# Optimization experiments

Hardware: AMD Instinct MI355X
Metric: run time of the kernel (lower is better)

## Reference

```python
import jax, jax.numpy as jnp
import numpy as np

N_ATOMS = 64
N_SAMPLES = 2 ** 15
SAMPLERATE = 22050
N_RES = 4096
N_ROOMS = 8
N_COEFFS = N_SAMPLES // 2 + 1


def make_waves():
    # musical_scale_hz(21, 106, 4096//4) -> 4 waveform families (sine, saw, square, triangle)
    n_steps = N_RES // 4
    midi = np.linspace(21.0, 106.0, n_steps)
    f0 = 440.0 * 2.0 ** ((midi - 69.0) / 12.0)
    rps = ((f0 / (SAMPLERATE / 2.0)) * np.pi).astype(np.float32)
    rad = rps[:, None] * np.arange(N_SAMPLES, dtype=np.float32)[None, :]
    sine = np.sin(rad)
    t = rad / (2.0 * np.pi)
    saw = (2.0 * (t - np.floor(t + 0.5))).astype(np.float32)
    sq = np.sign(sine).astype(np.float32)
    tri = (2.0 * np.abs(saw) - 1.0).astype(np.float32)
    return jnp.asarray(np.concatenate([sine, saw, sq, tri], 0).reshape(1, N_RES, N_SAMPLES))


def pdf2(means, stds, n):
    # gaussian pdf evaluated on linspace(0,1,n); means/stds: (1, A)
    rng = jnp.linspace(0.0, 1.0, n)
    mu = means[..., None]
    sd = stds[..., None]
    return jnp.exp(-0.5 * ((rng - mu) / sd) ** 2) / (sd * jnp.sqrt(2.0 * jnp.pi))


def linear_interp(x, n_out):
    # F.interpolate(mode='linear', align_corners=False) on last axis; x: (b, a, f)
    f = x.shape[-1]
    pos = (jnp.arange(n_out) + 0.5) * (f / n_out) - 0.5
    pos = jnp.clip(pos, 0.0, f - 1)
    i0 = jnp.floor(pos).astype(jnp.int32)
    i1 = jnp.minimum(i0 + 1, f - 1)
    w = (pos - i0).astype(x.dtype)
    return x[..., i0] * (1.0 - w) + x[..., i1] * w


def exponential_decay(decay_values, n_atoms, n_frames, base_resonance, n_samples):
    dv = jax.nn.sigmoid(decay_values.reshape(-1, n_atoms, 1))
    dv = jnp.broadcast_to(dv, (dv.shape[0], n_atoms, n_frames))
    decay = base_resonance + dv * (1.0 - base_resonance) * 0.95
    decay = jnp.exp(jnp.cumsum(jnp.log(decay + 1e-12), axis=-1))
    return linear_interp(decay, n_samples)


def fft_convolve(a, b):
    # zero-pad to 2N, multiply spectra, take first N samples
    n = a.shape[-1]
    pa = jnp.pad(a, ((0, 0), (0, 0), (0, n)))
    pb = jnp.pad(b, ((0, 0), (0, 0), (0, n)))
    spec = jnp.fft.rfft(pa, axis=-1) * jnp.fft.rfft(pb, axis=-1)
    return jnp.fft.irfft(spec, n=2 * n, axis=-1)[..., :n]


def layer_norm(x, w, b, eps=1e-5):
    m = jnp.mean(x, axis=-1, keepdims=True)
    v = jnp.var(x, axis=-1, keepdims=True)
    return (x - m) / jnp.sqrt(v + eps) * w + b


def sparse_softmax_st(x):
    soft = jax.nn.softmax(x, axis=-1)
    hard = jax.nn.one_hot(jnp.argmax(x, axis=-1), x.shape[-1], dtype=x.dtype)
    return hard + soft - jax.lax.stop_gradient(soft)


def model_forward(x, mix, decays, filter_decays, resonance_choice, noise_filter,
                  resonance_filter, resonance_filter2, env, amplitudes, verb_params,
                  noise, waves, ln_w, ln_b, mix_w1, mix_w2, room_w1, room_w2, room_irs):
    overall_mix = jax.nn.softmax(mix, axis=-1)                                   # (1,A,2)
    resonances = jnp.einsum('bar,brn->ban', jax.nn.relu(resonance_choice), waves)  # (1,A,N)

    # band-pass filtered noise (gaussian filter in frequency domain)
    noise_spec = jnp.fft.rfft(noise, axis=-1)
    noise_filt = pdf2(noise_filter[:, :, 0], jnp.abs(noise_filter[:, :, 1]) + 1e-12, N_COEFFS)
    filtered_noise = jnp.fft.irfft(noise_spec * noise_filt, n=N_SAMPLES, axis=-1)

    res_spec = jnp.fft.rfft(resonances, axis=-1)
    rf1 = pdf2(jnp.zeros_like(resonance_filter[:, :, 0]),
               jnp.abs(resonance_filter[:, :, 1]) + 1e-12, N_COEFFS)
    filtered_resonance = jnp.fft.irfft(res_spec * rf1, n=N_SAMPLES, axis=-1)
    rf2 = pdf2(jnp.zeros_like(resonance_filter2[:, :, 0]),
               jnp.abs(resonance_filter2[:, :, 1]) + 1e-12, N_COEFFS)
    filt_res_2 = jnp.fft.irfft(res_spec * rf2, n=N_SAMPLES, axis=-1)

    filt_crossfade = exponential_decay(filter_decays, N_ATOMS, 128, 0.02, N_SAMPLES)
    decay_env = exponential_decay(decays, N_ATOMS, 128, 0.02, N_SAMPLES)
    decaying_resonance = filtered_resonance * decay_env
    decaying_resonance2 = filt_res_2 * decay_env

    # gaussian envelope branch (gaussian_envelope = True)
    envelopes = pdf2(env[:, :, 0], jnp.abs(env[:, :, 1] + 1e-12) * 0.1, N_SAMPLES)
    positioned_noise = filtered_noise * envelopes

    res = fft_convolve(positioned_noise, decaying_resonance)
    res2 = fft_convolve(positioned_noise, decaying_resonance2)
    mixed = filt_crossfade * res + (1.0 - filt_crossfade) * res2

    final = positioned_noise * overall_mix[:, :, 0:1] + mixed * overall_mix[:, :, 1:2]
    final = final / (jnp.linalg.norm(final, axis=-1, keepdims=True) + 1e-8)
    amps = jnp.abs(amplitudes)
    final = final * amps

    # ReverbGenerator: layernorm -> small MLPs -> hard room choice -> fft convolve with IR
    h = layer_norm(verb_params, ln_w, ln_b)
    mix_v = jax.nn.sigmoid(jax.nn.leaky_relu(h @ mix_w1) @ mix_w2)               # (1,A,1)
    room_logits = jax.nn.leaky_relu(h @ room_w1) @ room_w2                        # (1,A,R)
    room = sparse_softmax_st(room_logits)
    ir = jnp.einsum('bar,rn->ban', room, room_irs)
    wet = fft_convolve(final, ir)
    out = final * mix_v + wet * (1.0 - mix_v)
    return out, amps


def setup_inputs() -> dict:
    key = jax.random.key(0)
    ks = jax.random.split(key, 20)
    return {
        'x': jax.random.normal(ks[0], (1, 1), jnp.float32),
        'mix': jax.random.uniform(ks[1], (1, N_ATOMS, 2), jnp.float32),
        'decays': jax.random.uniform(ks[2], (1, N_ATOMS, 1), jnp.float32, -6.0, 6.0),
        'filter_decays': jax.random.uniform(ks[3], (1, N_ATOMS, 1), jnp.float32, -6.0, 6.0),
        'resonance_choice': jax.random.uniform(ks[4], (1, N_ATOMS, N_RES), jnp.float32),
        'noise_filter': jax.random.uniform(ks[5], (1, N_ATOMS, 2), jnp.float32),
        'resonance_filter': jax.random.uniform(ks[6], (1, N_ATOMS, 2), jnp.float32),
        'resonance_filter2': jax.random.uniform(ks[7], (1, N_ATOMS, 2), jnp.float32),
        'env': jax.random.uniform(ks[8], (1, N_ATOMS, 2), jnp.float32),
        'amplitudes': jax.random.uniform(ks[9], (1, N_ATOMS, 1), jnp.float32) ** 2,
        'verb_params': jax.random.uniform(ks[10], (1, N_ATOMS, 4), jnp.float32, -1.0, 1.0),
        'noise': jax.random.uniform(ks[11], (1, N_ATOMS, N_SAMPLES), jnp.float32, -1.0, 1.0),
        'waves': make_waves(),
        'ln_w': jnp.ones((4,), jnp.float32),
        'ln_b': jnp.zeros((4,), jnp.float32),
        'mix_w1': jax.random.normal(ks[12], (4, 4), jnp.float32) * 0.1,
        'mix_w2': jax.random.normal(ks[13], (4, 1), jnp.float32) * 0.1,
        'room_w1': jax.random.normal(ks[14], (4, 4), jnp.float32) * 0.1,
        'room_w2': jax.random.normal(ks[15], (4, N_ROOMS), jnp.float32) * 0.1,
        'room_irs': jax.random.normal(ks[16], (N_ROOMS, N_SAMPLES), jnp.float32) * 0.01,
    }


def reference(x, mix, decays, filter_decays, resonance_choice, noise_filter,
              resonance_filter, resonance_filter2, env, amplitudes, verb_params,
              noise, waves, ln_w, ln_b, mix_w1, mix_w2, room_w1, room_w2, room_irs):
    return model_forward(x, mix, decays, filter_decays, resonance_choice, noise_filter,
                         resonance_filter, resonance_filter2, env, amplitudes, verb_params,
                         noise, waves, ln_w, ln_b, mix_w1, mix_w2, room_w1, room_w2, room_irs)
```

## Files before the change

kernel.cpp:

```cpp
#include <hip/hip_runtime.h>


typedef __attribute__((ext_vector_type(8))) short bf16x8;
typedef __attribute__((ext_vector_type(4))) float f32x4;

constexpr int SC_OM0   = 0;
constexpr int SC_OM1   = 64;
constexpr int SC_NFMU  = 128;
constexpr int SC_NFSD  = 192;
constexpr int SC_RF1SD = 256;
constexpr int SC_RF2SD = 320;
constexpr int SC_ENVMU = 384;
constexpr int SC_ENVSD = 448;
constexpr int SC_AMPS  = 512;
constexpr int SC_MIXV  = 576;
constexpr int SC_S0    = 640;
constexpr int SC_S1    = 704;
constexpr int SC_FSCALE= 768;
constexpr int SC_ROOM  = 832;
constexpr int SC_PSS   = 1024;
constexpr int SC_DTAB  = 4096;
constexpr int SC_FTAB  = 12288;

constexpr size_t OFF_SCAL = 0;
constexpr size_t OFF_CT   = 65536;
constexpr size_t OFF_P    = 327680;
constexpr size_t OFF_DS   = 8716288;
constexpr size_t OFF_RP   = OFF_DS;
constexpr size_t OFF_W64  = 17104896;
constexpr size_t OFF_NSS  = OFF_W64;
constexpr size_t OFF_W2   = OFF_W64 + 4194304;
constexpr size_t OFF_RSS  = 25493504;
constexpr size_t OFF_FINU = OFF_RSS;
constexpr size_t OFF_W1   = 29687808;
constexpr size_t OFF_FN   = 38076416;
constexpr size_t OFF_FR1  = 40173568;
constexpr size_t OFF_FR2  = 42270720;
constexpr size_t OFF_IRS  = 44367872;
constexpr size_t WS_FLOATS= 45416448;

__device__ __forceinline__ float2 cmul(float2 a, float2 b) {
  return make_float2(a.x*b.x - a.y*b.y, a.x*b.y + a.y*b.x);
}

__device__ __forceinline__ short f2bf(float x) {
  unsigned u = __float_as_uint(x);
  u = (u + 0x7FFFu + ((u >> 16) & 1u)) >> 16;
  return (short)u;
}

__device__ __forceinline__ void dft16(float2 d[16], float ei)
{
  const float CA[4] = {1.0f, 0.92387953251128674f, 0.70710678118654752f, 0.38268343236508977f};
  const float SA[4] = {0.0f, 0.38268343236508977f, 0.70710678118654752f, 0.92387953251128674f};
  const float CB[4] = {1.0f, 0.70710678118654752f, 0.0f, -0.70710678118654752f};
  const float SB[4] = {0.0f, 0.70710678118654752f, 1.0f, 0.70710678118654752f};
  float2 e[16];
  #pragma unroll
  for (int q = 0; q < 4; ++q) {
    float2 x0 = d[q], x1 = d[q+4], x2 = d[q+8], x3 = d[q+12];
    float ca = CA[q], sa = ei*SA[q], cb = CB[q], sb = ei*SB[q];
    float2 sum1 = make_float2(x0.x+x2.x, x0.y+x2.y);
    float2 d1   = make_float2(x0.x-x2.x, x0.y-x2.y);
    float2 dif1 = make_float2(d1.x*ca - d1.y*sa, d1.x*sa + d1.y*ca);
    float2 sum2 = make_float2(x1.x+x3.x, x1.y+x3.y);
    float2 d2   = make_float2(x1.x-x3.x, x1.y-x3.y);
    float2 dt   = make_float2(d2.x*ca - d2.y*sa, d2.x*sa + d2.y*ca);
    float2 dif2 = make_float2(-ei*dt.y, ei*dt.x);
    float2 Dm   = make_float2(sum1.x-sum2.x, sum1.y-sum2.y);
    float2 Dm2  = make_float2(dif1.x-dif2.x, dif1.y-dif2.y);
    e[4*q+0] = make_float2(sum1.x+sum2.x, sum1.y+sum2.y);
    e[4*q+1] = make_float2(dif1.x+dif2.x, dif1.y+dif2.y);
    e[4*q+2] = make_float2(Dm.x*cb - Dm.y*sb, Dm.x*sb + Dm.y*cb);
    e[4*q+3] = make_float2(Dm2.x*cb - Dm2.y*sb, Dm2.x*sb + Dm2.y*cb);
  }
  #pragma unroll
  for (int q = 0; q < 4; ++q) {
    float2 x0 = e[q], x1 = e[q+4], x2 = e[q+8], x3 = e[q+12];
    float2 sum1 = make_float2(x0.x+x2.x, x0.y+x2.y);
    float2 dif1 = make_float2(x0.x-x2.x, x0.y-x2.y);
    float2 sum2 = make_float2(x1.x+x3.x, x1.y+x3.y);
    float2 d2   = make_float2(x1.x-x3.x, x1.y-x3.y);
    float2 dif2 = make_float2(-ei*d2.y, ei*d2.x);
    d[q]    = make_float2(sum1.x+sum2.x, sum1.y+sum2.y);
    d[q+4]  = make_float2(dif1.x+dif2.x, dif1.y+dif2.y);
    d[q+8]  = make_float2(sum1.x-sum2.x, sum1.y-sum2.y);
    d[q+12] = make_float2(dif1.x-dif2.x, dif1.y-dif2.y);
  }
}

__device__ __forceinline__ void twiddleB(float2 d[16], int u, float dir2pi)
{
  float sn1, cs1;
  __sincosf(dir2pi * ((float)u * (1.0f/256.0f)), &sn1, &cs1);
  float2 w1 = make_float2(cs1, sn1);
  float2 tw = w1;
  #pragma unroll
  for (int k = 1; k < 16; ++k) { d[k] = cmul(d[k], tw); tw = cmul(tw, w1); }
}

template<int LEN>
__device__ float2* lds_fft(float2* src, float2* dst,
                           const float2* __restrict__ T256,
                           float dsign, float ei)
{
  constexpr int QB  = LEN >> 2;
  constexpr int FPT = (16 * QB) >> 8;
  constexpr int NST = (LEN == 256) ? 4 : 3;
  int n = LEN, s = 1, ls = 0;
  int sh = (LEN == 256) ? 0 : 1;

  if (LEN == 128) {
    constexpr int HB = LEN >> 1;
    constexpr int BPT = (16 * HB) >> 8;
    __syncthreads();
    #pragma unroll
    for (int b = 0; b < BPT; ++b) {
      int g = threadIdx.x + (b << 8);
      int row = g / HB;
      int beta = g & (HB - 1);
      float2 tj = T256[beta << 1];
      float cs = tj.x, sn = dsign * tj.y;
      float2 av = src[row*LEN + (beta ^ row)];
      float2 bv = src[row*LEN + ((beta + HB) ^ row)];
      float2 sum = make_float2(av.x + bv.x, av.y + bv.y);
      float2 dif = make_float2(av.x - bv.x, av.y - bv.y);
      float2 tw  = make_float2(dif.x*cs - dif.y*sn, dif.x*sn + dif.y*cs);
      dst[row*LEN + ((2*beta)     ^ row)] = sum;
      dst[row*LEN + ((2*beta + 1) ^ row)] = tw;
    }
    float2* t = src; src = dst; dst = t;
    n = 64; s = 2; ls = 1; sh = 2;
  }

  for (int st = 0; st < NST; ++st) {
    __syncthreads();
    #pragma unroll
    for (int b = 0; b < FPT; ++b) {
      int g   = threadIdx.x + (b << 8);
      int row = g / QB;
      int q   = g & (QB - 1);
      int p1  = q >> ls;
      int blo = q & (s - 1);
      int base = row * LEN;
      float2 x0 = src[base + ( q         ^ row)];
      float2 x1 = src[base + ((q +   QB) ^ row)];
      float2 x2 = src[base + ((q + 2*QB) ^ row)];
      float2 x3 = src[base + ((q + 3*QB) ^ row)];
      float2 tA = T256[p1 << sh];
      float caA = tA.x, saA = dsign * tA.y;
      float2 tB = T256[p1 << (sh + 1)];
      float caB = tB.x, saB = dsign * tB.y;
      float2 sum1 = make_float2(x0.x + x2.x, x0.y + x2.y);
      float2 d1   = make_float2(x0.x - x2.x, x0.y - x2.y);
      float2 dif1 = make_float2(d1.x*caA - d1.y*saA, d1.x*saA + d1.y*caA);
      float2 sum2 = make_float2(x1.x + x3.x, x1.y + x3.y);
      float2 d2   = make_float2(x1.x - x3.x, x1.y - x3.y);
      float2 dt   = make_float2(d2.x*caA - d2.y*saA, d2.x*saA + d2.y*caA);
      float2 dif2 = make_float2(-ei * dt.y, ei * dt.x);
      float2 S  = make_float2(sum1.x + sum2.x, sum1.y + sum2.y);
      float2 Dm = make_float2(sum1.x - sum2.x, sum1.y - sum2.y);
      float2 D  = make_float2(Dm.x*caB - Dm.y*saB, Dm.x*saB + Dm.y*caB);
      float2 S2 = make_float2(dif1.x + dif2.x, dif1.y + dif2.y);
      float2 Dm2= make_float2(dif1.x - dif2.x, dif1.y - dif2.y);
      float2 D2 = make_float2(Dm2.x*caB - Dm2.y*saB, Dm2.x*saB + Dm2.y*caB);
      int w0 = (p1 << (ls + 2)) | blo;
      dst[base + ( w0          ^ row)] = S;
      dst[base + ((w0 +     s) ^ row)] = S2;
      dst[base + ((w0 + 2 * s) ^ row)] = D;
      dst[base + ((w0 + 3 * s) ^ row)] = D2;
    }
    float2* t = src; src = dst; dst = t;
    n >>= 2; s <<= 2; ls += 2; sh += 2;
  }
  __syncthreads();
  return src;
}

template<int N1, int MODE_IN, int MODE_OUT>
__global__ __launch_bounds__(256) void k_fft_strided(
    float2* cbuf, const float* __restrict__ rin, const float* __restrict__ rin2,
    float* __restrict__ rout, float* __restrict__ rout2,
    const float* __restrict__ scal, const float* __restrict__ finU,
    float dir2pi, float outScale)
{
  constexpr int N  = N1 * 256;
  constexpr int NH = N >> 1;
  constexpr int LOG2N1 = (N1 == 256) ? 8 : 7;
  __shared__ float2 X[16*16*17];
  __shared__ float2 T256[256];
  __shared__ float2 TN[N1];
  __shared__ float red[256];
  const int a = blockIdx.y;
  const int n1base = blockIdx.x << 4;
  const int r = threadIdx.x & 15;
  const int u = threadIdx.x >> 4;
  const float ei = (dir2pi < 0.0f) ? -1.0f : 1.0f;

  if (MODE_OUT == 0) {
    float ang = dir2pi * ((float)threadIdx.x * (1.0f/256.0f));
    float sn, cs; __sincosf(ang, &sn, &cs);
    T256[threadIdx.x] = make_float2(cs, sn);
    if (threadIdx.x < N1) {
      float ang2 = dir2pi * ((float)threadIdx.x * (1.0f/(float)N));
      float sn2, cs2; __sincosf(ang2, &sn2, &cs2);
      TN[threadIdx.x] = make_float2(cs2, sn2);
    }
  }

  float sc = 1.0f;
  if (MODE_IN == 4) sc = scal[SC_FSCALE + a];
  float emu = 0.f, esd = 1.f, egp = 0.f;
  if (MODE_IN == 6 || MODE_OUT == 6) {
    emu = scal[SC_ENVMU + a];
    esd = scal[SC_ENVSD + a];
    egp = 0.3989422804014327f / esd;
  }
  float om0 = 0.f, om1 = 0.f;
  if (MODE_OUT == 6) { om0 = scal[SC_OM0 + a]; om1 = scal[SC_OM1 + a]; }

  float2 d[16];
  #pragma unroll
  for (int m = 0; m < 16; ++m) {
    int j = u + (m << 4);
    int n = n1base + r + N1 * j;
    float2 v;
    if (MODE_IN == 0) {
      v = cbuf[(size_t)a * N + n];
    } else if (MODE_IN == 3 || MODE_IN == 4) {
      float x = (n < NH) ? rin[(size_t)a * NH + n] * sc : 0.0f;
      v = make_float2(x, 0.0f);
    } else if (MODE_IN == 8) {
      v = make_float2(0.0f, 0.0f);
      if (n < NH) {
        float pos = ((float)n + 0.5f) * (1.0f/256.0f) - 0.5f;
        pos = fminf(fmaxf(pos, 0.0f), 127.0f);
        int i0 = (int)pos;
        float w = pos - (float)i0;
        int i1 = (i0 + 1 < 127) ? i0 + 1 : 127;
        const float* dt = scal + SC_DTAB + a*128;
        float de = dt[i0]*(1.0f-w) + dt[i1]*w;
        v = make_float2(rin[(size_t)a * NH + n] * de,
                        rin2[(size_t)a * NH + n] * de);
      }
    } else {
      float x = 0.0f;
      if (n < NH) {
        float uu = (float)n * (1.0f / 32767.0f);
        float te = (uu - emu) / esd;
        float envv = __expf(-0.5f * te * te) * egp;
        x = rin[(size_t)a * NH + n] * envv;
      }
      v = make_float2(x, 0.0f);
    }
    d[m] = v;
  }

  dft16(d, ei);
  twiddleB(d, u, dir2pi);
  #pragma unroll
  for (int k = 0; k < 16; ++k) X[(u*16 + k)*17 + r] = d[k];
  __syncthreads();
  #pragma unroll
  for (int m = 0; m < 16; ++m) d[m] = X[(m*16 + u)*17 + r];
  dft16(d, ei);

  float ss = 0.0f;
  #pragma unroll
  for (int k1 = 0; k1 < 16; ++k1) {
    int j = u + (k1 << 4);
    float2 v = d[k1];
    int n = n1base + r + N1 * j;
    if (MODE_OUT == 0) {
      int aa = (n1base + r) * j;
      float2 tw = cmul(T256[(aa >> LOG2N1) & 255], TN[aa & (N1 - 1)]);
      cbuf[(size_t)a * N + n] = cmul(v, tw);
    } else if (MODE_OUT == 3) {
      if (n < NH) {
        float w0 = scal[SC_S0 + a], w1 = scal[SC_S1 + a];
        rout[(size_t)a * NH + n] =
            v.x * outScale * w1 + finU[(size_t)a * NH + n] * w0;
      }
    } else {
      if (n < NH) {
        float resv  = v.x * outScale;
        float res2v = v.y * outScale;
        float uu = (float)n * (1.0f / 32767.0f);
        float te = (uu - emu) / esd;
        float envv = __expf(-0.5f * te * te) * egp;
        float pnv = rin[(size_t)a * NH + n] * envv;
        float pos = ((float)n + 0.5f) * (1.0f/256.0f) - 0.5f;
        pos = fminf(fmaxf(pos, 0.0f), 127.0f);
        int i0 = (int)pos;
        float w = pos - (float)i0;
        int i1 = (i0 + 1 < 127) ? i0 + 1 : 127;
        const float* ft = scal + SC_FTAB + a*128;
        float fc = ft[i0]*(1.0f-w) + ft[i1]*w;
        float f = pnv*om0 + (fc*resv + (1.0f-fc)*res2v)*om1;
        rout[(size_t)a * NH + n] = f;
        ss += f * f;
      }
    }
  }

  if (MODE_OUT == 6) {
    red[threadIdx.x] = ss;
    __syncthreads();
    for (int s = 128; s > 0; s >>= 1) {
      if (threadIdx.x < s) red[threadIdx.x] += red[threadIdx.x + s];
      __syncthreads();
    }
    if (threadIdx.x == 0) rout2[SC_PSS + a*16 + blockIdx.x] = red[0];
  }
}

__global__ __launch_bounds__(256) void k_fft_s128_first(
    float2* __restrict__ RSs, float2* __restrict__ NSs,
    const float* __restrict__ rez, const float* __restrict__ noise)
{
  constexpr int N1 = 128, N = 32768;
  constexpr float FWD = -6.283185307179586f;
  __shared__ float2 X[16*16*17];
  __shared__ float2 T256[256];
  __shared__ float2 TN[128];
  const bool isRS = blockIdx.y < 64;
  const int a = isRS ? blockIdx.y : blockIdx.y - 64;
  const int n1base = blockIdx.x << 4;
  const int r = threadIdx.x & 15;
  const int u = threadIdx.x >> 4;

  {
    float ang = FWD * ((float)threadIdx.x * (1.0f/256.0f));
    float sn, cs; __sincosf(ang, &sn, &cs);
    T256[threadIdx.x] = make_float2(cs, sn);
    if (threadIdx.x < 128) {
      float ang2 = FWD * ((float)threadIdx.x * (1.0f/(float)N));
      float sn2, cs2; __sincosf(ang2, &sn2, &cs2);
      TN[threadIdx.x] = make_float2(cs2, sn2);
    }
  }

  float2 d[16];
  #pragma unroll
  for (int m = 0; m < 16; ++m) {
    int j = u + (m << 4);
    int n = n1base + r + N1 * j;
    float x = isRS ? (rez[(size_t)a * N + n] + rez[(size_t)(64 + a) * N + n])
                   : noise[(size_t)a * N + n];
    d[m] = make_float2(x, 0.0f);
  }

  dft16(d, -1.0f);
  twiddleB(d, u, FWD);
  #pragma unroll
  for (int k = 0; k < 16; ++k) X[(u*16 + k)*17 + r] = d[k];
  __syncthreads();
  #pragma unroll
  for (int m = 0; m < 16; ++m) d[m] = X[(m*16 + u)*17 + r];
  dft16(d, -1.0f);

  float2* outp = isRS ? RSs : NSs;
  #pragma unroll
  for (int k1 = 0; k1 < 16; ++k1) {
    int j = u + (k1 << 4);
    int n = n1base + r + N1 * j;
    int aa = (n1base + r) * j;
    float2 tw = cmul(T256[(aa >> 7) & 255], TN[aa & 127]);
    outp[(size_t)a * N + n] = cmul(d[k1], tw);
  }
}

__global__ __launch_bounds__(256) void k_fft_m128_both(
    const float2* __restrict__ RSs, const float2* __restrict__ NSs,
    float2* __restrict__ W1, float2* __restrict__ W2,
    const float* __restrict__ scal)
{
  constexpr int N1 = 128;
  constexpr int N = N1 * 256;
  constexpr int ITERS = (16 * N1) >> 8;
  constexpr int LOG2N1 = 7;
  constexpr float FWD = -6.283185307179586f;
  constexpr float IVD = +6.283185307179586f;
  __shared__ float2 A[16 * N1];
  __shared__ float2 B[16 * N1];
  __shared__ float2 T256[256];
  __shared__ float2 TN[N1];
  const bool isRS = blockIdx.y < 64;
  const int a = isRS ? blockIdx.y : blockIdx.y - 64;
  const int colbase = blockIdx.x << 4;

  {
    float ang = FWD * ((float)threadIdx.x * (1.0f/256.0f));
    float sn, cs; __sincosf(ang, &sn, &cs);
    T256[threadIdx.x] = make_float2(cs, sn);
    if (threadIdx.x < N1) {
      float ang2 = IVD * ((float)threadIdx.x * (1.0f/(float)N));
      float sn2, cs2; __sincosf(ang2, &sn2, &cs2);
      TN[threadIdx.x] = make_float2(cs2, sn2);
    }
  }

  float mu = 0.f, isd1 = 0.f, g1 = 0.f, isd2 = 0.f, g2 = 0.f;
  if (isRS) {
    float s1 = scal[SC_RF1SD + a], s2 = scal[SC_RF2SD + a];
    isd1 = 1.0f/s1; g1 = 0.3989422804014327f/s1;
    isd2 = 1.0f/s2; g2 = 0.3989422804014327f/s2;
  } else {
    float sd = scal[SC_NFSD + a]; mu = scal[SC_NFMU + a];
    isd1 = 1.0f/sd; g1 = 0.3989422804014327f/sd;
  }
  const float2* zin = (isRS ? RSs : NSs) + (size_t)a * N;
  float2* out = (isRS ? W1 : W2) + (size_t)a * N;

  #pragma unroll
  for (int it = 0; it < ITERS; ++it) {
    int flat = threadIdx.x + (it << 8);
    int c = flat / N1, j = flat & (N1 - 1);
    A[c*N1 + (j ^ c)] = zin[(size_t)(colbase + c) * N1 + j];
  }
  float2* cur = lds_fft<N1>(A, B, T256, 1.0f, -1.0f);
  float2* alt = (cur == A) ? B : A;

  #pragma unroll
  for (int it = 0; it < ITERS; ++it) {
    int flat = threadIdx.x + (it << 8);
    int c = flat / N1, j = flat & (N1 - 1);
    int idx = c*N1 + (j ^ c);
    float2 v = cur[idx];
    int k  = (colbase + c) + (j << 8);
    int kk = (k <= N - k) ? k : N - k;
    if (isRS) {
      float fr = (float)kk * (2.0f/(float)N);
      float t1 = fr * isd1, t2 = fr * isd2;
      float ga = __expf(-0.5f * t1 * t1) * g1;
      float gb = __expf(-0.5f * t2 * t2) * g2;
      v = make_float2(v.x*ga - v.y*gb, v.x*gb + v.y*ga);
    } else {
      float t = ((float)kk * (2.0f/(float)N) - mu) * isd1;
      float g = __expf(-0.5f * t * t) * g1;
      v.x *= g; v.y *= g;
    }
    cur[idx] = v;
  }

  float2* r2 = lds_fft<N1>(cur, alt, T256, -1.0f, 1.0f);

  #pragma unroll
  for (int it = 0; it < ITERS; ++it) {
    int flat = threadIdx.x + (it << 8);
    int c = flat / N1, j = flat & (N1 - 1);
    float2 v = r2[c*N1 + (j ^ c)];
    int aa = j * (colbase + c);
    float2 t1 = T256[(aa >> LOG2N1) & 255];
    t1.y = -t1.y;
    float2 tw = cmul(t1, TN[aa & (N1 - 1)]);
    out[(size_t)(colbase + c) * N1 + j] = cmul(v, tw);
  }
}

__global__ __launch_bounds__(256) void k_fft_s128_last(
    const float2* __restrict__ W1, const float2* __restrict__ W2,
    float* __restrict__ fr1, float* __restrict__ fr2, float* __restrict__ fn)
{
  constexpr int N1 = 128, N = 32768;
  constexpr float IVD = +6.283185307179586f;
  constexpr float S32 = 1.0f / 32768.0f;
  __shared__ float2 X[16*16*17];
  const bool isRS = blockIdx.y < 64;
  const int a = isRS ? blockIdx.y : blockIdx.y - 64;
  const int n1base = blockIdx.x << 4;
  const int r = threadIdx.x & 15;
  const int u = threadIdx.x >> 4;

  const float2* cb = (isRS ? W1 : W2) + (size_t)a * N;
  float2 d[16];
  #pragma unroll
  for (int m = 0; m < 16; ++m) {
    int j = u + (m << 4);
    d[m] = cb[n1base + r + N1 * j];
  }
  dft16(d, 1.0f);
  twiddleB(d, u, IVD);
  #pragma unroll
  for (int k = 0; k < 16; ++k) X[(u*16 + k)*17 + r] = d[k];
  __syncthreads();
  #pragma unroll
  for (int m = 0; m < 16; ++m) d[m] = X[(m*16 + u)*17 + r];
  dft16(d, 1.0f);

  #pragma unroll
  for (int k1 = 0; k1 < 16; ++k1) {
    int j = u + (k1 << 4);
    int n = n1base + r + N1 * j;
    if (isRS) {
      fr1[(size_t)a * N + n] = d[k1].x * S32;
      fr2[(size_t)a * N + n] = d[k1].y * S32;
    } else {
      fn[(size_t)a * N + n] = d[k1].x * S32;
    }
  }
}

__global__ __launch_bounds__(256) void k_fft_mid256dual(
    const float2* __restrict__ zin, const float2* __restrict__ zin2half,
    float2* __restrict__ out1, const int* __restrict__ roomArr)
{
  constexpr int N = 65536;
  constexpr float FWD = -6.283185307179586f;
  constexpr float IVD = +6.283185307179586f;
  __shared__ float2 X[16*16*17];
  __shared__ float2 T256[256];
  __shared__ float2 TN[256];
  const int a = blockIdx.y;
  const int colbase = blockIdx.x << 4;
  const int u  = threadIdx.x & 15;
  const int rc = threadIdx.x >> 4;

  {
    float ang = FWD * ((float)threadIdx.x * (1.0f/256.0f));
    float sn, cs; __sincosf(ang, &sn, &cs);
    T256[threadIdx.x] = make_float2(cs, sn);
    float ang2 = IVD * ((float)threadIdx.x * (1.0f/(float)N));
    float sn2, cs2; __sincosf(ang2, &sn2, &cs2);
    TN[threadIdx.x] = make_float2(cs2, sn2);
  }
  __syncthreads();

  const float2* z2 = zin2half + (size_t)(roomArr ? roomArr[a] : a) * N;
  const size_t rowG = (size_t)a * N + (size_t)(colbase + rc) * 256;
  const size_t rowZ2 = (size_t)(colbase + rc) * 256;

  float2 d[16];
  #pragma unroll
  for (int m = 0; m < 16; ++m) d[m] = zin[rowG + u + (m << 4)];
  dft16(d, -1.0f);
  twiddleB(d, u, FWD);
  #pragma unroll
  for (int k = 0; k < 16; ++k) X[(rc*16 + k)*17 + u] = d[k];
  #pragma unroll
  for (int m = 0; m < 16; ++m) d[m] = X[(rc*16 + u)*17 + m];
  dft16(d, -1.0f);

  float2 stash[16];
  #pragma unroll
  for (int k = 0; k < 16; ++k) stash[k] = d[k];
  #pragma unroll
  for (int m = 0; m < 16; ++m) d[m] = z2[rowZ2 + u + (m << 4)];
  dft16(d, -1.0f);
  twiddleB(d, u, FWD);
  #pragma unroll
  for (int k = 0; k < 16; ++k) X[(rc*16 + k)*17 + u] = d[k];
  #pragma unroll
  for (int m = 0; m < 16; ++m) d[m] = X[(rc*16 + u)*17 + m];
  dft16(d, -1.0f);
  #pragma unroll
  for (int k = 0; k < 16; ++k) d[k] = cmul(stash[k], d[k]);

  dft16(d, 1.0f);
  twiddleB(d, u, IVD);
  #pragma unroll
  for (int k = 0; k < 16; ++k) X[(rc*16 + k)*17 + u] = d[k];
  #pragma unroll
  for (int m = 0; m < 16; ++m) d[m] = X[(rc*16 + u)*17 + m];
  dft16(d, 1.0f);

  #pragma unroll
  for (int k1 = 0; k1 < 16; ++k1) {
    int j = u + (k1 << 4);
    int aa = j * (colbase + rc);
    float2 t1 = T256[(aa >> 8) & 255];
    t1.y = -t1.y;
    float2 tw = cmul(t1, TN[aa & 255]);
    out1[rowG + j] = cmul(d[k1], tw);
  }
}

__global__ void k_scalars(
    const float* __restrict__ mix, const float* __restrict__ decays,
    const float* __restrict__ fdec, const float* __restrict__ nf,
    const float* __restrict__ rf1, const float* __restrict__ rf2,
    const float* __restrict__ env, const float* __restrict__ amplitudes,
    const float* __restrict__ verb, const float* __restrict__ ln_w,
    const float* __restrict__ ln_b, const float* __restrict__ mw1,
    const float* __restrict__ mw2, const float* __restrict__ rw1,
    const float* __restrict__ rw2, float* __restrict__ scal,
    float* __restrict__ dout)
{
  int a = threadIdx.x;
  if (a >= 64) return;
  float m0 = mix[a*2+0], m1 = mix[a*2+1];
  float mx = fmaxf(m0, m1);
  float e0 = expf(m0 - mx), e1 = expf(m1 - mx);
  float inv = 1.0f / (e0 + e1);
  scal[SC_OM0+a] = e0 * inv;
  scal[SC_OM1+a] = e1 * inv;
  scal[SC_NFMU+a] = nf[a*2+0];
  scal[SC_NFSD+a] = fabsf(nf[a*2+1]) + 1e-12f;
  scal[SC_RF1SD+a] = fabsf(rf1[a*2+1]) + 1e-12f;
  scal[SC_RF2SD+a] = fabsf(rf2[a*2+1]) + 1e-12f;
  scal[SC_ENVMU+a] = env[a*2+0];
  scal[SC_ENVSD+a] = fabsf(env[a*2+1] + 1e-12f) * 0.1f;
  float amp = fabsf(amplitudes[a]);
  scal[SC_AMPS+a] = amp;
  dout[2097152 + a] = amp;
  float d  = 0.02f + (1.0f/(1.0f+expf(-decays[a]))) * (0.98f * 0.95f);
  float fd = 0.02f + (1.0f/(1.0f+expf(-fdec[a])))   * (0.98f * 0.95f);
  float pd = 1.0f, pf = 1.0f;
  for (int f = 0; f < 128; ++f) {
    pd *= d; pf *= fd;
    scal[SC_DTAB + a*128 + f] = pd;
    scal[SC_FTAB + a*128 + f] = pf;
  }
  float x0 = verb[a*4+0], x1 = verb[a*4+1], x2 = verb[a*4+2], x3 = verb[a*4+3];
  float mean = (x0+x1+x2+x3) * 0.25f;
  float d0 = x0-mean, d1 = x1-mean, d2 = x2-mean, d3 = x3-mean;
  float var = (d0*d0 + d1*d1 + d2*d2 + d3*d3) * 0.25f;
  float rs = 1.0f / sqrtf(var + 1e-5f);
  float h[4] = { d0*rs*ln_w[0]+ln_b[0], d1*rs*ln_w[1]+ln_b[1],
                 d2*rs*ln_w[2]+ln_b[2], d3*rs*ln_w[3]+ln_b[3] };
  float t[4], u[4];
  for (int j = 0; j < 4; ++j) {
    float s1 = 0.f, s2 = 0.f;
    for (int i2 = 0; i2 < 4; ++i2) {
      s1 += h[i2] * mw1[i2*4 + j];
      s2 += h[i2] * rw1[i2*4 + j];
    }
    t[j] = (s1 > 0.f) ? s1 : 0.01f*s1;
    u[j] = (s2 > 0.f) ? s2 : 0.01f*s2;
  }
  float ml = 0.f;
  for (int j = 0; j < 4; ++j) ml += t[j] * mw2[j];
  scal[SC_MIXV+a] = 1.0f / (1.0f + expf(-ml));
  float best = -1e30f; int bi = 0;
  for (int r = 0; r < 8; ++r) {
    float lg = 0.f;
    for (int j = 0; j < 4; ++j) lg += u[j] * rw2[j*8 + r];
    if (lg > best) { best = lg; bi = r; }
  }
  ((int*)scal)[SC_ROOM + a] = bi;
}

__global__ void k_packA(const float* __restrict__ rc, short* __restrict__ ctb)
{
  int o = blockIdx.x * 256 + threadIdx.x;
  int m = o >> 12, k = o & 4095;
  int s = k >> 2, f = k & 3;
  float v = fmaxf(rc[m*4096 + f*1024 + s], 0.0f);
  ctb[o] = f2bf(v);
}

__global__ __launch_bounds__(512) void k_gemm_mfma(
    const float* __restrict__ waves, const short* __restrict__ ctb,
    float* __restrict__ rp)
{
  const int t = threadIdx.x;
  const int w = t >> 6, lane = t & 63;
  const int ml = lane & 15, q = lane >> 4;
  const int col = blockIdx.x * 128 + w * 16 + ml;
  const int part = blockIdx.y;
  const int kb0 = part * 64;

  f32x4 acc[4] = {};

  const float* ws0 = waves + (size_t)(kb0*8 + 2*q) * 32768 + col;
  const float* ws1 = waves + (size_t)(1024 + kb0*8 + 2*q) * 32768 + col;
  const short* abase = ctb + (size_t)ml * 4096 + (size_t)kb0 * 32 + q * 8;

  #define LOADW(v, kbl) { size_t o = (size_t)(kbl) * (8*32768); \
    v[0] = ws0[o]; v[1] = ws0[o + 32768]; v[2] = ws1[o]; v[3] = ws1[o + 32768]; }

  #define DOKB(v, kbl) { \
    float sq0 = (v[0] > 0.f) ? 1.f : ((v[0] < 0.f) ? -1.f : v[0]); \
    float sq1 = (v[1] > 0.f) ? 1.f : ((v[1] < 0.f) ? -1.f : v[1]); \
    float tr0 = 2.f * fabsf(v[2]) - 1.f; \
    float tr1 = 2.f * fabsf(v[3]) - 1.f; \
    bf16x8 b; \
    b[0] = f2bf(v[0]); b[1] = f2bf(v[2]); b[2] = f2bf(sq0); b[3] = f2bf(tr0); \
    b[4] = f2bf(v[1]); b[5] = f2bf(v[3]); b[6] = f2bf(sq1); b[7] = f2bf(tr1); \
    const short* ap = abase + (size_t)(kbl) * 32; \
    acc[0] = __builtin_amdgcn_mfma_f32_16x16x32_bf16(*(const bf16x8*)(ap),                      b, acc[0], 0,0,0); \
    acc[1] = __builtin_amdgcn_mfma_f32_16x16x32_bf16(*(const bf16x8*)(ap + (size_t)16*4096),    b, acc[1], 0,0,0); \
    acc[2] = __builtin_amdgcn_mfma_f32_16x16x32_bf16(*(const bf16x8*)(ap + (size_t)32*4096),    b, acc[2], 0,0,0); \
    acc[3] = __builtin_amdgcn_mfma_f32_16x16x32_bf16(*(const bf16x8*)(ap + (size_t)48*4096),    b, acc[3], 0,0,0); }

  float vA[4], vB[4];
  LOADW(vA, 0);
  LOADW(vB, 1);
  for (int kbl = 0; kbl < 64; kbl += 2) {
    DOKB(vA, kbl);
    if (kbl + 2 < 64) LOADW(vA, kbl + 2);
    DOKB(vB, kbl + 1);
    if (kbl + 3 < 64) LOADW(vB, kbl + 3);
  }
  #undef LOADW
  #undef DOKB

  #pragma unroll
  for (int mt = 0; mt < 4; ++mt) {
    #pragma unroll
    for (int rr = 0; rr < 4; ++rr) {
      rp[(size_t)(part*64 + mt*16 + q*4 + rr) * 32768 + col] = acc[mt][rr];
    }
  }
}

__global__ void k_norm(float* __restrict__ scal)
{
  int a = threadIdx.x;
  if (a >= 64) return;
  float ss = 0.0f;
  for (int i = 0; i < 16; ++i) ss += scal[SC_PSS + a*16 + i];
  float s = scal[SC_AMPS+a] / (sqrtf(ss) + 1e-8f);
  float mixv = scal[SC_MIXV+a];
  scal[SC_FSCALE+a] = s;
  scal[SC_S0+a] = s * mixv;
  scal[SC_S1+a] = 1.0f - mixv;
}

extern "C" void kernel_launch(void* const* d_in, const int* in_sizes, int n_in,
                              void* d_out, int out_size, void* d_ws, size_t ws_size,
                              hipStream_t stream)
{
  const float* mix   = (const float*)d_in[1];
  const float* dec   = (const float*)d_in[2];
  const float* fdec  = (const float*)d_in[3];
  const float* rc    = (const float*)d_in[4];
  const float* nf    = (const float*)d_in[5];
  const float* rf1   = (const float*)d_in[6];
  const float* rf2   = (const float*)d_in[7];
  const float* env   = (const float*)d_in[8];
  const float* amps  = (const float*)d_in[9];
  const float* verb  = (const float*)d_in[10];
  const float* noise = (const float*)d_in[11];
  const float* waves = (const float*)d_in[12];
  const float* lnw   = (const float*)d_in[13];
  const float* lnb   = (const float*)d_in[14];
  const float* mw1   = (const float*)d_in[15];
  const float* mw2   = (const float*)d_in[16];
  const float* rw1   = (const float*)d_in[17];
  const float* rw2   = (const float*)d_in[18];
  const float* rirs  = (const float*)d_in[19];
  float* out = (float*)d_out;
  float* w   = (float*)d_ws;

  if (ws_size < WS_FLOATS * 4ULL) return;

  float*  scal = w + OFF_SCAL;
  short*  ctb  = (short*)(w + OFF_CT);
  float*  rp   = w + OFF_RP;
  float2* P    = (float2*)(w + OFF_P);
  float2* Ds   = (float2*)(w + OFF_DS);
  float2* W64  = (float2*)(w + OFF_W64);
  float2* RSs  = (float2*)(w + OFF_RSS);
  float2* NSs  = (float2*)(w + OFF_NSS);
  float2* W2   = (float2*)(w + OFF_W2);
  float*  finU = w + OFF_FINU;
  float2* W1   = (float2*)(w + OFF_W1);
  float*  fn   = w + OFF_FN;
  float*  fr1  = w + OFF_FR1;
  float*  fr2  = w + OFF_FR2;
  float2* IRS  = (float2*)(w + OFF_IRS);
  const int* room = ((const int*)(w + OFF_SCAL)) + SC_ROOM;

  const float FWD = -6.283185307179586f;
  const float INV = +6.283185307179586f;
  const float S64 = 1.0f / 65536.0f;

  k_scalars<<<1, 64, 0, stream>>>(mix, dec, fdec, nf, rf1, rf2, env, amps, verb,
                                  lnw, lnb, mw1, mw2, rw1, rw2, scal, out);
  k_packA<<<1024, 256, 0, stream>>>(rc, ctb);
  k_gemm_mfma<<<dim3(256, 2), 512, 0, stream>>>(waves, ctb, rp);

  k_fft_strided<256,3,0><<<dim3(16,8),256,0,stream>>>(IRS, rirs, nullptr, nullptr, nullptr, scal, nullptr, FWD, 1.f);

  k_fft_s128_first<<<dim3(8,128),256,0,stream>>>(RSs, NSs, rp, noise);
  k_fft_m128_both<<<dim3(16,128),256,0,stream>>>(RSs, NSs, W1, W2, scal);
  k_fft_s128_last<<<dim3(8,128),256,0,stream>>>(W1, W2, fr1, fr2, fn);

  k_fft_strided<256,6,0><<<dim3(16,64),256,0,stream>>>(P, fn, nullptr, nullptr, nullptr, scal, nullptr, FWD, 1.f);

  k_fft_strided<256,8,0><<<dim3(16,64),256,0,stream>>>(Ds, fr1, fr2, nullptr, nullptr, scal, nullptr, FWD, 1.f);
  k_fft_mid256dual<<<dim3(16,64),256,0,stream>>>(Ds, P, W64, nullptr);
  k_fft_strided<256,0,6><<<dim3(16,64),256,0,stream>>>(W64, fn, nullptr, finU, scal, scal, nullptr, INV, S64);

  k_norm<<<1,64,0,stream>>>(scal);

  k_fft_strided<256,4,0><<<dim3(16,64),256,0,stream>>>(Ds, finU, nullptr, nullptr, nullptr, scal, nullptr, FWD, 1.f);
  k_fft_mid256dual<<<dim3(16,64),256,0,stream>>>(Ds, IRS, W64, room);
  k_fft_strided<256,0,3><<<dim3(16,64),256,0,stream>>>(W64, nullptr, nullptr, out, nullptr, scal, finU, INV, S64);
}
```

Measured before the change: 319.8 us.

## Fuse inverse FFT with next forward pass, merge Ds/P FFTs, drop norm kernel

```diff
diff --git a/kernel.cpp b/kernel.cpp
--- a/kernel.cpp
+++ b/kernel.cpp
@@ -14,9 +14,6 @@
 constexpr int SC_ENVSD = 448;
 constexpr int SC_AMPS  = 512;
 constexpr int SC_MIXV  = 576;
-constexpr int SC_S0    = 640;
-constexpr int SC_S1    = 704;
-constexpr int SC_FSCALE= 768;
 constexpr int SC_ROOM  = 832;
 constexpr int SC_PSS   = 1024;
 constexpr int SC_DTAB  = 4096;
@@ -190,14 +187,13 @@
   __shared__ float2 X[16*16*17];
   __shared__ float2 T256[256];
   __shared__ float2 TN[N1];
-  __shared__ float red[256];
   const int a = blockIdx.y;
   const int n1base = blockIdx.x << 4;
   const int r = threadIdx.x & 15;
   const int u = threadIdx.x >> 4;
   const float ei = (dir2pi < 0.0f) ? -1.0f : 1.0f;
 
-  if (MODE_OUT == 0) {
+  {
     float ang = dir2pi * ((float)threadIdx.x * (1.0f/256.0f));
     float sn, cs; __sincosf(ang, &sn, &cs);
     T256[threadIdx.x] = make_float2(cs, sn);
@@ -208,31 +204,74 @@
     }
   }
 
-  float sc = 1.0f;
-  if (MODE_IN == 4) sc = scal[SC_FSCALE + a];
+  float2 d[16];
+  #pragma unroll
+  for (int m = 0; m < 16; ++m) {
+    int j = u + (m << 4);
+    int n = n1base + r + N1 * j;
+    float x = (n < NH) ? rin[(size_t)a * NH + n] : 0.0f;
+    d[m] = make_float2(x, 0.0f);
+  }
+
+  dft16(d, ei);
+  twiddleB(d, u, dir2pi);
+  #pragma unroll
+  for (int k = 0; k < 16; ++k) X[(u*16 + k)*17 + r] = d[k];
+  __syncthreads();
+  #pragma unroll
+  for (int m = 0; m < 16; ++m) d[m] = X[(m*16 + u)*17 + r];
+  dft16(d, ei);
+
+  #pragma unroll
+  for (int k1 = 0; k1 < 16; ++k1) {
+    int j = u + (k1 << 4);
+    int n = n1base + r + N1 * j;
+    int aa = (n1base + r) * j;
+    float2 tw = cmul(T256[(aa >> LOG2N1) & 255], TN[aa & (N1 - 1)]);
+    cbuf[(size_t)a * N + n] = cmul(d[k1], tw);
+  }
+}
+
+__global__ __launch_bounds__(256) void k_fft_s256_DsP(
+    float2* __restrict__ Ds, float2* __restrict__ P,
+    const float* __restrict__ fr1, const float* __restrict__ fr2,
+    const float* __restrict__ fn, const float* __restrict__ scal)
+{
+  constexpr int N = 65536, NH = 32768;
+  constexpr float FWD = -6.283185307179586f;
+  __shared__ float2 X[16*16*17];
+  __shared__ float2 T256[256];
+  __shared__ float2 TN[256];
+  const bool isDs = blockIdx.y < 64;
+  const int a = isDs ? blockIdx.y : blockIdx.y - 64;
+  const int n1base = blockIdx.x << 4;
+  const int r = threadIdx.x & 15;
+  const int u = threadIdx.x >> 4;
+
+  {
+    float ang = FWD * ((float)threadIdx.x * (1.0f/256.0f));
+    float sn, cs; __sincosf(ang, &sn, &cs);
+    T256[threadIdx.x] = make_float2(cs, sn);
+    float ang2 = FWD * ((float)threadIdx.x * (1.0f/(float)N));
+    float sn2, cs2; __sincosf(ang2, &sn2, &cs2);
+    TN[threadIdx.x] = make_float2(cs2, sn2);
+  }
+
   float emu = 0.f, esd = 1.f, egp = 0.f;
-  if (MODE_IN == 6 || MODE_OUT == 6) {
+  if (!isDs) {
     emu = scal[SC_ENVMU + a];
     esd = scal[SC_ENVSD + a];
     egp = 0.3989422804014327f / esd;
   }
-  float om0 = 0.f, om1 = 0.f;
-  if (MODE_OUT == 6) { om0 = scal[SC_OM0 + a]; om1 = scal[SC_OM1 + a]; }
 
   float2 d[16];
   #pragma unroll
   for (int m = 0; m < 16; ++m) {
     int j = u + (m << 4);
-    int n = n1base + r + N1 * j;
-    float2 v;
-    if (MODE_IN == 0) {
-      v = cbuf[(size_t)a * N + n];
-    } else if (MODE_IN == 3 || MODE_IN == 4) {
-      float x = (n < NH) ? rin[(size_t)a * NH + n] * sc : 0.0f;
-      v = make_float2(x, 0.0f);
-    } else if (MODE_IN == 8) {
-      v = make_float2(0.0f, 0.0f);
-      if (n < NH) {
+    int n = n1base + r + 256 * j;
+    float2 v = make_float2(0.0f, 0.0f);
+    if (n < NH) {
+      if (isDs) {
         float pos = ((float)n + 0.5f) * (1.0f/256.0f) - 0.5f;
         pos = fminf(fmaxf(pos, 0.0f), 127.0f);
         int i0 = (int)pos;
@@ -240,77 +279,35 @@
         int i1 = (i0 + 1 < 127) ? i0 + 1 : 127;
         const float* dt = scal + SC_DTAB + a*128;
         float de = dt[i0]*(1.0f-w) + dt[i1]*w;
-        v = make_float2(rin[(size_t)a * NH + n] * de,
-                        rin2[(size_t)a * NH + n] * de);
-      }
-    } else {
-      float x = 0.0f;
-      if (n < NH) {
+        v = make_float2(fr1[(size_t)a * NH + n] * de,
+                        fr2[(size_t)a * NH + n] * de);
+      } else {
         float uu = (float)n * (1.0f / 32767.0f);
         float te = (uu - emu) / esd;
         float envv = __expf(-0.5f * te * te) * egp;
-        x = rin[(size_t)a * NH + n] * envv;
+        v = make_float2(fn[(size_t)a * NH + n] * envv, 0.0f);
       }
-      v = make_float2(x, 0.0f);
     }
     d[m] = v;
   }
 
-  dft16(d, ei);
-  twiddleB(d, u, dir2pi);
+  dft16(d, -1.0f);
+  twiddleB(d, u, FWD);
   #pragma unroll
   for (int k = 0; k < 16; ++k) X[(u*16 + k)*17 + r] = d[k];
   __syncthreads();
   #pragma unroll
   for (int m = 0; m < 16; ++m) d[m] = X[(m*16 + u)*17 + r];
-  dft16(d, ei);
-
-  float ss = 0.0f;
+  dft16(d, -1.0f);
+
+  float2* outp = isDs ? Ds : P;
   #pragma unroll
   for (int k1 = 0; k1 < 16; ++k1) {
     int j = u + (k1 << 4);
-    float2 v = d[k1];
-    int n = n1base + r + N1 * j;
-    if (MODE_OUT == 0) {
-      int aa = (n1base + r) * j;
-      float2 tw = cmul(T256[(aa >> LOG2N1) & 255], TN[aa & (N1 - 1)]);
-      cbuf[(size_t)a * N + n] = cmul(v, tw);
-    } else if (MODE_OUT == 3) {
-      if (n < NH) {
-        float w0 = scal[SC_S0 + a], w1 = scal[SC_S1 + a];
-        rout[(size_t)a * NH + n] =
-            v.x * outScale * w1 + finU[(size_t)a * NH + n] * w0;
-      }
-    } else {
-      if (n < NH) {
-        float resv  = v.x * outScale;
-        float res2v = v.y * outScale;
-        float uu = (float)n * (1.0f / 32767.0f);
-        float te = (uu - emu) / esd;
-        float envv = __expf(-0.5f * te * te) * egp;
-        float pnv = rin[(size_t)a * NH + n] * envv;
-        float pos = ((float)n + 0.5f) * (1.0f/256.0f) - 0.5f;
-        pos = fminf(fmaxf(pos, 0.0f), 127.0f);
-        int i0 = (int)pos;
-        float w = pos - (float)i0;
-        int i1 = (i0 + 1 < 127) ? i0 + 1 : 127;
-        const float* ft = scal + SC_FTAB + a*128;
-        float fc = ft[i0]*(1.0f-w) + ft[i1]*w;
-        float f = pnv*om0 + (fc*resv + (1.0f-fc)*res2v)*om1;
-        rout[(size_t)a * NH + n] = f;
-        ss += f * f;
-      }
-    }
-  }
-
-  if (MODE_OUT == 6) {
-    red[threadIdx.x] = ss;
-    __syncthreads();
-    for (int s = 128; s > 0; s >>= 1) {
-      if (threadIdx.x < s) red[threadIdx.x] += red[threadIdx.x + s];
-      __syncthreads();
-    }
-    if (threadIdx.x == 0) rout2[SC_PSS + a*16 + blockIdx.x] = red[0];
+    int n = n1base + r + 256 * j;
+    int aa = (n1base + r) * j;
+    float2 tw = cmul(T256[(aa >> 8) & 255], TN[aa & 255]);
+    outp[(size_t)a * N + n] = cmul(d[k1], tw);
   }
 }
 
@@ -345,8 +342,13 @@
   for (int m = 0; m < 16; ++m) {
     int j = u + (m << 4);
     int n = n1base + r + N1 * j;
-    float x = isRS ? (rez[(size_t)a * N + n] + rez[(size_t)(64 + a) * N + n])
-                   : noise[(size_t)a * N + n];
+    float x;
+    if (isRS) {
+      x = rez[(size_t)a * N + n] + rez[(size_t)(64 + a) * N + n]
+        + rez[(size_t)(128 + a) * N + n] + rez[(size_t)(192 + a) * N + n];
+    } else {
+      x = noise[(size_t)a * N + n];
+    }
     d[m] = make_float2(x, 0.0f);
   }
 
@@ -572,6 +574,150 @@
     t1.y = -t1.y;
     float2 tw = cmul(t1, TN[aa & 255]);
     out1[rowG + j] = cmul(d[k1], tw);
+  }
+}
+
+__global__ __launch_bounds__(256) void k_fft_out6fwd(
+    const float2* __restrict__ W64in, const float* __restrict__ fn,
+    float* __restrict__ finU, float* __restrict__ scal,
+    float2* __restrict__ DsOut)
+{
+  constexpr int N = 65536, NH = 32768;
+  constexpr float FWD = -6.283185307179586f;
+  constexpr float IVD = +6.283185307179586f;
+  constexpr float S64 = 1.0f / 65536.0f;
+  __shared__ float2 X[16*16*17];
+  __shared__ float2 T256[256];
+  __shared__ float2 TN[256];
+  __shared__ float red[256];
+  const int a = blockIdx.y;
+  const int n1base = blockIdx.x << 4;
+  const int r = threadIdx.x & 15;
+  const int u = threadIdx.x >> 4;
+
+  {
+    float ang = FWD * ((float)threadIdx.x * (1.0f/256.0f));
+    float sn, cs; __sincosf(ang, &sn, &cs);
+    T256[threadIdx.x] = make_float2(cs, sn);
+    float ang2 = FWD * ((float)threadIdx.x * (1.0f/(float)N));
+    float sn2, cs2; __sincosf(ang2, &sn2, &cs2);
+    TN[threadIdx.x] = make_float2(cs2, sn2);
+  }
+
+  const float emu = scal[SC_ENVMU + a];
+  const float esd = scal[SC_ENVSD + a];
+  const float egp = 0.3989422804014327f / esd;
+  const float om0 = scal[SC_OM0 + a], om1 = scal[SC_OM1 + a];
+  const float* ft = scal + SC_FTAB + a*128;
+
+  float2 d[16];
+  #pragma unroll
+  for (int m = 0; m < 16; ++m) {
+    int j = u + (m << 4);
+    d[m] = W64in[(size_t)a * N + n1base + r + 256 * j];
+  }
+  dft16(d, 1.0f);
+  twiddleB(d, u, IVD);
+  #pragma unroll
+  for (int k = 0; k < 16; ++k) X[(u*16 + k)*17 + r] = d[k];
+  __syncthreads();
+  #pragma unroll
+  for (int m = 0; m < 16; ++m) d[m] = X[(m*16 + u)*17 + r];
+  dft16(d, 1.0f);
+
+  float fv[8];
+  float ss = 0.0f;
+  #pragma unroll
+  for (int k1 = 0; k1 < 8; ++k1) {
+    int n = n1base + r + 256 * (u + (k1 << 4));
+    float resv  = d[k1].x * S64;
+    float res2v = d[k1].y * S64;
+    float uu = (float)n * (1.0f / 32767.0f);
+    float te = (uu - emu) / esd;
+    float envv = __expf(-0.5f * te * te) * egp;
+    float pnv = fn[(size_t)a * NH + n] * envv;
+    float pos = ((float)n + 0.5f) * (1.0f/256.0f) - 0.5f;
+    pos = fminf(fmaxf(pos, 0.0f), 127.0f);
+    int i0 = (int)pos;
+    float w = pos - (float)i0;
+    int i1 = (i0 + 1 < 127) ? i0 + 1 : 127;
+    float fc = ft[i0]*(1.0f-w) + ft[i1]*w;
+    float f = pnv*om0 + (fc*resv + (1.0f-fc)*res2v)*om1;
+    finU[(size_t)a * NH + n] = f;
+    fv[k1] = f;
+    ss += f * f;
+  }
+  red[threadIdx.x] = ss;
+  __syncthreads();
+  for (int s = 128; s > 0; s >>= 1) {
+    if (threadIdx.x < s) red[threadIdx.x] += red[threadIdx.x + s];
+    __syncthreads();
+  }
+  if (threadIdx.x == 0) scal[SC_PSS + a*16 + blockIdx.x] = red[0];
+
+  #pragma unroll
+  for (int m = 0; m < 16; ++m)
+    d[m] = (m < 8) ? make_float2(fv[m], 0.0f) : make_float2(0.0f, 0.0f);
+  dft16(d, -1.0f);
+  twiddleB(d, u, FWD);
+  #pragma unroll
+  for (int k = 0; k < 16; ++k) X[(u*16 + k)*17 + r] = d[k];
+  __syncthreads();
+  #pragma unroll
+  for (int m = 0; m < 16; ++m) d[m] = X[(m*16 + u)*17 + r];
+  dft16(d, -1.0f);
+
+  #pragma unroll
+  for (int k1 = 0; k1 < 16; ++k1) {
+    int j = u + (k1 << 4);
+    int n = n1base + r + 256 * j;
+    int aa = (n1base + r) * j;
+    float2 tw = cmul(T256[(aa >> 8) & 255], TN[aa & 255]);
+    DsOut[(size_t)a * N + n] = cmul(d[k1], tw);
+  }
+}
+
+__global__ __launch_bounds__(256) void k_fft_s256_out3(
+    const float2* __restrict__ W64in, const float* __restrict__ finU,
+    const float* __restrict__ scal, float* __restrict__ out)
+{
+  constexpr int N = 65536, NH = 32768;
+  constexpr float IVD = +6.283185307179586f;
+  constexpr float S64 = 1.0f / 65536.0f;
+  __shared__ float2 X[16*16*17];
+  const int a = blockIdx.y;
+  const int n1base = blockIdx.x << 4;
+  const int r = threadIdx.x & 15;
+  const int u = threadIdx.x >> 4;
+
+  float ss = 0.0f;
+  #pragma unroll
+  for (int i = 0; i < 16; ++i) ss += scal[SC_PSS + a*16 + i];
+  float fscale = scal[SC_AMPS + a] / (sqrtf(ss) + 1e-8f);
+  float mixv = scal[SC_MIXV + a];
+  float w1 = fscale * (1.0f - mixv);
+  float w0 = fscale * mixv;
+
+  float2 d[16];
+  #pragma unroll
+  for (int m = 0; m < 16; ++m) {
+    int j = u + (m << 4);
+    d[m] = W64in[(size_t)a * N + n1base + r + 256 * j];
+  }
+  dft16(d, 1.0f);
+  twiddleB(d, u, IVD);
+  #pragma unroll
+  for (int k = 0; k < 16; ++k) X[(u*16 + k)*17 + r] = d[k];
+  __syncthreads();
+  #pragma unroll
+  for (int m = 0; m < 16; ++m) d[m] = X[(m*16 + u)*17 + r];
+  dft16(d, 1.0f);
+
+  #pragma unroll
+  for (int k1 = 0; k1 < 8; ++k1) {
+    int n = n1base + r + 256 * (u + (k1 << 4));
+    out[(size_t)a * NH + n] =
+        d[k1].x * S64 * w1 + finU[(size_t)a * NH + n] * w0;
   }
 }
 
@@ -658,13 +804,12 @@
   const int ml = lane & 15, q = lane >> 4;
   const int col = blockIdx.x * 128 + w * 16 + ml;
   const int part = blockIdx.y;
-  const int kb0 = part * 64;
 
   f32x4 acc[4] = {};
 
-  const float* ws0 = waves + (size_t)(kb0*8 + 2*q) * 32768 + col;
-  const float* ws1 = waves + (size_t)(1024 + kb0*8 + 2*q) * 32768 + col;
-  const short* abase = ctb + (size_t)ml * 4096 + (size_t)kb0 * 32 + q * 8;
+  const float* ws0 = waves + (size_t)(part*256 + 2*q) * 32768 + col;
+  const float* ws1 = waves + (size_t)(1024 + part*256 + 2*q) * 32768 + col;
+  const short* abase = ctb + (size_t)ml * 4096 + (size_t)part * 1024 + q * 8;
 
   #define LOADW(v, kbl) { size_t o = (size_t)(kbl) * (8*32768); \
     v[0] = ws0[o]; v[1] = ws0[o + 32768]; v[2] = ws1[o]; v[3] = ws1[o + 32768]; }
@@ -678,19 +823,19 @@
     b[0] = f2bf(v[0]); b[1] = f2bf(v[2]); b[2] = f2bf(sq0); b[3] = f2bf(tr0); \
     b[4] = f2bf(v[1]); b[5] = f2bf(v[3]); b[6] = f2bf(sq1); b[7] = f2bf(tr1); \
     const short* ap = abase + (size_t)(kbl) * 32; \
-    acc[0] = __builtin_amdgcn_mfma_f32_16x16x32_bf16(*(const bf16x8*)(ap),                      b, acc[0], 0,0,0); \
-    acc[1] = __builtin_amdgcn_mfma_f32_16x16x32_bf16(*(const bf16x8*)(ap + (size_t)16*4096),    b, acc[1], 0,0,0); \
-    acc[2] = __builtin_amdgcn_mfma_f32_16x16x32_bf16(*(const bf16x8*)(ap + (size_t)32*4096),    b, acc[2], 0,0,0); \
-    acc[3] = __builtin_amdgcn_mfma_f32_16x16x32_bf16(*(const bf16x8*)(ap + (size_t)48*4096),    b, acc[3], 0,0,0); }
+    acc[0] = __builtin_amdgcn_mfma_f32_16x16x32_bf16(*(const bf16x8*)(ap),                   b, acc[0], 0,0,0); \
+    acc[1] = __builtin_amdgcn_mfma_f32_16x16x32_bf16(*(const bf16x8*)(ap + (size_t)16*4096), b, acc[1], 0,0,0); \
+    acc[2] = __builtin_amdgcn_mfma_f32_16x16x32_bf16(*(const bf16x8*)(ap + (size_t)32*4096), b, acc[2], 0,0,0); \
+    acc[3] = __builtin_amdgcn_mfma_f32_16x16x32_bf16(*(const bf16x8*)(ap + (size_t)48*4096), b, acc[3], 0,0,0); }
 
   float vA[4], vB[4];
   LOADW(vA, 0);
   LOADW(vB, 1);
-  for (int kbl = 0; kbl < 64; kbl += 2) {
+  for (int kbl = 0; kbl < 32; kbl += 2) {
     DOKB(vA, kbl);
-    if (kbl + 2 < 64) LOADW(vA, kbl + 2);
+    if (kbl + 2 < 32) LOADW(vA, kbl + 2);
     DOKB(vB, kbl + 1);
-    if (kbl + 3 < 64) LOADW(vB, kbl + 3);
+    if (kbl + 3 < 32) LOADW(vB, kbl + 3);
   }
   #undef LOADW
   #undef DOKB
@@ -702,19 +847,6 @@
       rp[(size_t)(part*64 + mt*16 + q*4 + rr) * 32768 + col] = acc[mt][rr];
     }
   }
-}
-
-__global__ void k_norm(float* __restrict__ scal)
-{
-  int a = threadIdx.x;
-  if (a >= 64) return;
-  float ss = 0.0f;
-  for (int i = 0; i < 16; ++i) ss += scal[SC_PSS + a*16 + i];
-  float s = scal[SC_AMPS+a] / (sqrtf(ss) + 1e-8f);
-  float mixv = scal[SC_MIXV+a];
-  scal[SC_FSCALE+a] = s;
-  scal[SC_S0+a] = s * mixv;
-  scal[SC_S1+a] = 1.0f - mixv;
 }
 
 extern "C" void kernel_launch(void* const* d_in, const int* in_sizes, int n_in,
@@ -763,13 +895,11 @@
   const int* room = ((const int*)(w + OFF_SCAL)) + SC_ROOM;
 
   const float FWD = -6.283185307179586f;
-  const float INV = +6.283185307179586f;
-  const float S64 = 1.0f / 65536.0f;
 
   k_scalars<<<1, 64, 0, stream>>>(mix, dec, fdec, nf, rf1, rf2, env, amps, verb,
                                   lnw, lnb, mw1, mw2, rw1, rw2, scal, out);
   k_packA<<<1024, 256, 0, stream>>>(rc, ctb);
-  k_gemm_mfma<<<dim3(256, 2), 512, 0, stream>>>(waves, ctb, rp);
+  k_gemm_mfma<<<dim3(256, 4), 512, 0, stream>>>(waves, ctb, rp);
 
   k_fft_strided<256,3,0><<<dim3(16,8),256,0,stream>>>(IRS, rirs, nullptr, nullptr, nullptr, scal, nullptr, FWD, 1.f);
 
@@ -777,15 +907,13 @@
   k_fft_m128_both<<<dim3(16,128),256,0,stream>>>(RSs, NSs, W1, W2, scal);
   k_fft_s128_last<<<dim3(8,128),256,0,stream>>>(W1, W2, fr1, fr2, fn);
 
-  k_fft_strided<256,6,0><<<dim3(16,64),256,0,stream>>>(P, fn, nullptr, nullptr, nullptr, scal, nullptr, FWD, 1.f);
-
-  k_fft_strided<256,8,0><<<dim3(16,64),256,0,stream>>>(Ds, fr1, fr2, nullptr, nullptr, scal, nullptr, FWD, 1.f);
+  k_fft_s256_DsP<<<dim3(16,128),256,0,stream>>>(Ds, P, fr1, fr2, fn, scal);
+
   k_fft_mid256dual<<<dim3(16,64),256,0,stream>>>(Ds, P, W64, nullptr);
-  k_fft_strided<256,0,6><<<dim3(16,64),256,0,stream>>>(W64, fn, nullptr, finU, scal, scal, nullptr, INV, S64);
-
-  k_norm<<<1,64,0,stream>>>(scal);
-
-  k_fft_strided<256,4,0><<<dim3(16,64),256,0,stream>>>(Ds, finU, nullptr, nullptr, nullptr, scal, nullptr, FWD, 1.f);
+
+  k_fft_out6fwd<<<dim3(16,64),256,0,stream>>>(W64, fn, finU, scal, Ds);
+
   k_fft_mid256dual<<<dim3(16,64),256,0,stream>>>(Ds, IRS, W64, room);
-  k_fft_strided<256,0,3><<<dim3(16,64),256,0,stream>>>(W64, nullptr, nullptr, out, nullptr, scal, finU, INV, S64);
-}
+
+  k_fft_s256_out3<<<dim3(16,64),256,0,stream>>>(W64, finU, scal, out);
+}
```

Measured after the change: 332.8 us. 1.04x slower.
